# Optimization experiments

Measured on AMD Instinct MI355X. Metric: run time of the kernel, lower is better.

## Reference

```python
import jax, jax.numpy as jnp
from jax import lax
import numpy as np

B, T, NCLS, D = 64, 2048, 20, 2048
LCS_LEN, FSD_LEN = 64, 32
LAMB1, LAMB2, LAMB3 = 1.0, 5e-5, 8e-5
LAMB_LCS, LAMB_FSD = 0.01, 0.01
FEAT_MARGIN = 50.0
THRES = 0.5
GAMMA = 0.1


def cos_sim(a, b):
    a = a / jnp.linalg.norm(a, axis=1, keepdims=True)
    b = b / jnp.linalg.norm(b, axis=1, keepdims=True)
    return a @ b.T


def dp_fsd(c0, c1):
    # soft-LCS/DTW-style recurrence with maxGamma (soft max) over 3 neighbors
    h = c0.shape[-1] // 2
    m = cos_sim(c0[:, :h], c1[:, :h])  # [L, L]
    g = cos_sim(c0[:, h:], c1[:, h:])  # [L, L]
    L = m.shape[0]

    def row_step(prev_row, mg):
        m_row, g_row = mg
        diag = prev_row[:-1]  # C[i-1, j-1]
        up = prev_row[1:]     # C[i-1, j]

        def col_step(left, xs):  # left = C[i, j-1]
            d, u, mij, gij = xs
            neigh = jnp.stack([d, gij + u, gij + left])
            val = mij + GAMMA * jax.nn.logsumexp(neigh / GAMMA)
            return val, val

        _, row_vals = lax.scan(col_step, jnp.zeros((), m.dtype), (diag, up, m_row, g_row))
        new_row = jnp.concatenate([jnp.zeros((1,), m.dtype), row_vals])
        return new_row, None

    final_row, _ = lax.scan(row_step, jnp.zeros(L + 1, m.dtype), (m, g))
    return final_row[-1]


def dp_lcs(c0, c1):
    s = cos_sim(c0, c1)  # [L, L]
    L = s.shape[0]

    def row_step(prev_row, s_row):
        diag = prev_row[:-1]
        up = prev_row[1:]

        def col_step(left, xs):
            d, u, sij = xs
            val = jnp.where(sij > THRES, d + sij, jnp.maximum(u, left))
            return val, val

        _, row_vals = lax.scan(col_step, jnp.zeros((), s.dtype), (diag, up, s_row))
        return jnp.concatenate([jnp.zeros((1,), s.dtype), row_vals]), None

    final_row, _ = lax.scan(row_step, jnp.zeros(L + 1, s.dtype), s)
    return final_row[-1]


def cls_criterion(p, lab):
    return -jnp.mean(jnp.sum(jnp.log(p + 1e-10) * lab, axis=1))


def forward_once(ai_cls, ac_cls, ab_cls, vlab, att, ai_feat, ac_feat, ab_feat, ai_cas):
    bs = ai_cls.shape[0]
    ones = jnp.ones((bs, 1), ai_cls.dtype)
    zeros = jnp.zeros((bs, 1), ai_cls.dtype)
    inst_lab = jnp.concatenate([vlab, zeros], axis=1)
    cont_lab = jnp.concatenate([vlab, ones], axis=1)
    back_lab = jnp.concatenate([jnp.zeros_like(vlab), ones], axis=1)
    inst_lab = inst_lab / jnp.sum(inst_lab, axis=1, keepdims=True)
    cont_lab = cont_lab / jnp.sum(cont_lab, axis=1, keepdims=True)
    back_lab = back_lab / jnp.sum(back_lab, axis=1, keepdims=True)

    inst_loss = cls_criterion(ai_cls, inst_lab)
    cont_loss = cls_criterion(ac_cls, cont_lab)
    back_loss = cls_criterion(ab_cls, back_lab)

    guide_loss = jnp.mean(jnp.sum(jnp.abs(1.0 - ai_cas[:, :, -1] - lax.stop_gradient(att[:, :, 0])), axis=1))

    n_inst = jnp.linalg.norm(ai_feat, axis=1)
    n_cont = jnp.linalg.norm(ac_feat, axis=1)
    n_back = jnp.linalg.norm(ab_feat, axis=1)
    f1 = jnp.maximum(FEAT_MARGIN - n_inst + n_cont, 0.0)
    f2 = jnp.maximum(FEAT_MARGIN - n_cont + n_back, 0.0)
    f3 = n_back
    feat_loss = jnp.mean((f1 + f2 + f3) ** 2)

    sparse_loss = jnp.mean(jnp.sum(att[:, :, :2], axis=1))

    cls_loss = inst_loss + cont_loss + back_loss  # THUMOS14 weights 1/1/1
    return cls_loss + LAMB1 * guide_loss + LAMB2 * feat_loss + LAMB3 * sparse_loss


def _pair_loss(vals, pair_label):
    bs = vals.shape[0]
    pos = jnp.sum(vals * pair_label)
    neg = jnp.sum(vals * (1.0 - pair_label))
    pos_num = jnp.sum(pair_label)
    neg_num = bs - pos_num
    return neg / (neg_num + 1e-10) - pos / (pos_num + 1e-10)


def ftcl_forward(act_inst_cls_0, act_cont_cls_0, act_back_cls_0, vid_label_0, temp_att_0,
                 act_inst_feat_0, act_cont_feat_0, act_back_feat_0, act_inst_cas_0,
                 lcs_candi_0, fsd_act_candi_0, fsd_bak_candi_0,
                 act_inst_cls_1, act_cont_cls_1, act_back_cls_1, vid_label_1, temp_att_1,
                 act_inst_feat_1, act_cont_feat_1, act_back_feat_1, act_inst_cas_1,
                 lcs_candi_1, fsd_act_candi_1, fsd_bak_candi_1):
    loss_0 = forward_once(act_inst_cls_0, act_cont_cls_0, act_back_cls_0, vid_label_0, temp_att_0,
                          act_inst_feat_0, act_cont_feat_0, act_back_feat_0, act_inst_cas_0)
    loss_1 = forward_once(act_inst_cls_1, act_cont_cls_1, act_back_cls_1, vid_label_1, temp_att_1,
                          act_inst_feat_1, act_cont_feat_1, act_back_feat_1, act_inst_cas_1)
    acm_loss = (loss_0 + loss_1) / 2.0

    pair_label = (jnp.sum(vid_label_0 * vid_label_1, axis=1) > 0).astype(jnp.float32)  # [B]

    lcs = jax.vmap(dp_lcs)(lcs_candi_0, lcs_candi_1)  # [B]
    lcs_loss = _pair_loss(lcs, pair_label)

    # pair==1 -> act_1, pair==0 -> bak_1 (matches the per-sample branch in torch)
    fsd_c1 = jnp.where(pair_label[:, None, None] > 0, fsd_act_candi_1, fsd_bak_candi_1)
    fsd = jax.vmap(dp_fsd)(fsd_act_candi_0, fsd_c1)  # [B]
    fsd_loss = _pair_loss(fsd, pair_label)

    return acm_loss + LAMB_LCS * lcs_loss + LAMB_FSD * fsd_loss


def setup_inputs() -> dict:
    key = jax.random.key(0)
    ks = iter(jax.random.split(key, 32))
    rand = lambda s: jax.random.uniform(next(ks), s, jnp.float32)
    randn = lambda s: jax.random.normal(next(ks), s, jnp.float32)
    inp = {}
    for sfx in ('0', '1'):
        inp[f'act_inst_cls_{sfx}'] = rand((B, NCLS + 1))
        inp[f'act_cont_cls_{sfx}'] = rand((B, NCLS + 1))
        inp[f'act_back_cls_{sfx}'] = rand((B, NCLS + 1))
        inp[f'vid_label_{sfx}'] = jnp.ones((B, NCLS), jnp.float32)
        inp[f'temp_att_{sfx}'] = rand((B, T, 3))
        inp[f'act_inst_feat_{sfx}'] = randn((B, D))
        inp[f'act_cont_feat_{sfx}'] = randn((B, D))
        inp[f'act_back_feat_{sfx}'] = randn((B, D))
        inp[f'act_inst_cas_{sfx}'] = rand((B, T, NCLS + 1))
        inp[f'lcs_candi_{sfx}'] = randn((B, LCS_LEN, D))
        inp[f'fsd_act_candi_{sfx}'] = randn((B, FSD_LEN, D))
        inp[f'fsd_bak_candi_{sfx}'] = randn((B, FSD_LEN, D))
    return inp


def reference(act_inst_cls_0, act_cont_cls_0, act_back_cls_0, vid_label_0, temp_att_0,
              act_inst_feat_0, act_cont_feat_0, act_back_feat_0, act_inst_cas_0,
              lcs_candi_0, fsd_act_candi_0, fsd_bak_candi_0,
              act_inst_cls_1, act_cont_cls_1, act_back_cls_1, vid_label_1, temp_att_1,
              act_inst_feat_1, act_cont_feat_1, act_back_feat_1, act_inst_cas_1,
              lcs_candi_1, fsd_act_candi_1, fsd_bak_candi_1):
    return ftcl_forward(act_inst_cls_0, act_cont_cls_0, act_back_cls_0, vid_label_0, temp_att_0,
                        act_inst_feat_0, act_cont_feat_0, act_back_feat_0, act_inst_cas_0,
                        lcs_candi_0, fsd_act_candi_0, fsd_bak_candi_0,
                        act_inst_cls_1, act_cont_cls_1, act_back_cls_1, vid_label_1, temp_att_1,
                        act_inst_feat_1, act_cont_feat_1, act_back_feat_1, act_inst_cas_1,
                        lcs_candi_1, fsd_act_candi_1, fsd_bak_candi_1)
```

## Files before the change

### kernel.cpp

```cpp
#include <hip/hip_runtime.h>
#include <math.h>

#define Bn 64
#define Tn 2048
#define NCLS 20
#define Dn 2048
#define LCSL 64
#define FSDL 32

typedef __bf16 bf16x4 __attribute__((ext_vector_type(4)));
typedef __bf16 bf16x8 __attribute__((ext_vector_type(8)));
typedef float f32x4 __attribute__((ext_vector_type(4)));

#define WS_LCS 0
#define WS_FSD 64
#define WS_NORM 128
#define WS_GS 512
#define WS_LSQ 1024
#define WS_FSQ 66560
#define WS_SPART 99328
#define WS_MG 2196480

__global__ __launch_bounds__(256) void mega_kernel(
    const float* __restrict__ lcs0, const float* __restrict__ lcs1,
    const float* __restrict__ fA0, const float* __restrict__ fA1,
    const float* __restrict__ fB1,
    const float* __restrict__ vid0, const float* __restrict__ vid1,
    const float* __restrict__ cas0, const float* __restrict__ att0,
    const float* __restrict__ cas1, const float* __restrict__ att1,
    const float* __restrict__ f0, const float* __restrict__ f1,
    const float* __restrict__ f2, const float* __restrict__ f3,
    const float* __restrict__ f4, const float* __restrict__ f5,
    float* __restrict__ ws) {
    __shared__ __bf16 tA[4096];
    __shared__ __bf16 tB[4096];
    const int t = threadIdx.x;
    const int bid = blockIdx.x;
    const int w = t >> 6, lane = t & 63;
    const int quad = lane >> 4, l16 = lane & 15;

    if (bid < 512) {
        const int b = bid >> 3, ks = bid & 7;
        const float* c0 = lcs0 + (size_t)b * LCSL * Dn + ks * 256;
        const float* c1 = lcs1 + (size_t)b * LCSL * Dn + ks * 256;

        f32x4 acc[4] = {};
        float sqa[4] = {0.f, 0.f, 0.f, 0.f}, sqb[4] = {0.f, 0.f, 0.f, 0.f};
        float4 pA[4], pB[4];
        #pragma unroll
        for (int l = 0; l < 4; ++l) {
            int idx4 = l * 256 + t;
            int row = idx4 >> 4, kq4 = idx4 & 15;
            pA[l] = *(const float4*)(c0 + (size_t)row * Dn + kq4 * 4);
            pB[l] = *(const float4*)(c1 + (size_t)row * Dn + kq4 * 4);
        }
        for (int kc = 0; kc < 4; ++kc) {
            __syncthreads();
            #pragma unroll
            for (int l = 0; l < 4; ++l) {
                int idx4 = l * 256 + t;
                int row = idx4 >> 4, kq4 = idx4 & 15;
                int c = kq4 >> 1, h = kq4 & 1;
                int pos = row * 64 + ((c ^ (row & 7)) << 3) + h * 4;
                float4 av = pA[l], bv = pB[l];
                bf16x4 a4 = {(__bf16)av.x, (__bf16)av.y, (__bf16)av.z, (__bf16)av.w};
                bf16x4 b4 = {(__bf16)bv.x, (__bf16)bv.y, (__bf16)bv.z, (__bf16)bv.w};
                *(bf16x4*)&tA[pos] = a4;
                *(bf16x4*)&tB[pos] = b4;
                sqa[l] += av.x * av.x + av.y * av.y + av.z * av.z + av.w * av.w;
                sqb[l] += bv.x * bv.x + bv.y * bv.y + bv.z * bv.z + bv.w * bv.w;
            }
            if (kc < 3) {
                const float* n0 = c0 + (kc + 1) * 64;
                const float* n1 = c1 + (kc + 1) * 64;
                #pragma unroll
                for (int l = 0; l < 4; ++l) {
                    int idx4 = l * 256 + t;
                    int row = idx4 >> 4, kq4 = idx4 & 15;
                    pA[l] = *(const float4*)(n0 + (size_t)row * Dn + kq4 * 4);
                    pB[l] = *(const float4*)(n1 + (size_t)row * Dn + kq4 * 4);
                }
            }
            __syncthreads();
            #pragma unroll
            for (int s = 0; s < 2; ++s) {
                int ar = w * 16 + l16;
                int ac_ = (s * 4 + quad) ^ (ar & 7);
                bf16x8 af = *(const bf16x8*)&tA[ar * 64 + (ac_ << 3)];
                #pragma unroll
                for (int tj = 0; tj < 4; ++tj) {
                    int br = tj * 16 + l16;
                    int bc = (s * 4 + quad) ^ (br & 7);
                    bf16x8 bf = *(const bf16x8*)&tB[br * 64 + (bc << 3)];
                    acc[tj] = __builtin_amdgcn_mfma_f32_16x16x32_bf16(af, bf, acc[tj], 0, 0, 0);
                }
            }
        }
        float* dst = ws + WS_SPART + (size_t)(b * 8 + ks) * 4096;
        #pragma unroll
        for (int tj = 0; tj < 4; ++tj)
            #pragma unroll
            for (int rg = 0; rg < 4; ++rg)
                dst[(w * 16 + quad * 4 + rg) * 64 + tj * 16 + l16] = acc[tj][rg];
        #pragma unroll
        for (int l = 0; l < 4; ++l) {
            float sa = sqa[l], sb = sqb[l];
            #pragma unroll
            for (int m = 1; m < 16; m <<= 1) {
                sa += __shfl_xor(sa, m);
                sb += __shfl_xor(sb, m);
            }
            if ((t & 15) == 0) {
                int r = l * 16 + (t >> 4);
                float* q = ws + WS_LSQ + (size_t)(b * 8 + ks) * 128;
                q[r] = sa;
                q[64 + r] = sb;
            }
        }
    } else if (bid < 1024) {
        const int qb = bid - 512;
        const int b = qb >> 3, half = (qb >> 2) & 1, ks = qb & 3;
        float ps = 0.f;
        for (int c = 0; c < NCLS; ++c) ps += vid0[b * NCLS + c] * vid1[b * NCLS + c];
        const float* base1 = (ps > 0.f) ? fA1 : fB1;
        const float* c0 = fA0 + (size_t)b * FSDL * Dn + half * 1024 + ks * 256;
        const float* c1 = base1 + (size_t)b * FSDL * Dn + half * 1024 + ks * 256;
        const int wi = w >> 1, wj = w & 1;

        f32x4 acc = {};
        float sqa[2] = {0.f, 0.f}, sqb[2] = {0.f, 0.f};
        float4 pA[2], pB[2];
        #pragma unroll
        for (int l = 0; l < 2; ++l) {
            int idx4 = l * 256 + t;
            int row = idx4 >> 4, kq4 = idx4 & 15;
            pA[l] = *(const float4*)(c0 + (size_t)row * Dn + kq4 * 4);
            pB[l] = *(const float4*)(c1 + (size_t)row * Dn + kq4 * 4);
        }
        for (int kc = 0; kc < 4; ++kc) {
            __syncthreads();
            #pragma unroll
            for (int l = 0; l < 2; ++l) {
                int idx4 = l * 256 + t;
                int row = idx4 >> 4, kq4 = idx4 & 15;
                int c = kq4 >> 1, h = kq4 & 1;
                int pos = row * 64 + ((c ^ (row & 7)) << 3) + h * 4;
                float4 av = pA[l], bv = pB[l];
                bf16x4 a4 = {(__bf16)av.x, (__bf16)av.y, (__bf16)av.z, (__bf16)av.w};
                bf16x4 b4 = {(__bf16)bv.x, (__bf16)bv.y, (__bf16)bv.z, (__bf16)bv.w};
                *(bf16x4*)&tA[pos] = a4;
                *(bf16x4*)&tB[pos] = b4;
                sqa[l] += av.x * av.x + av.y * av.y + av.z * av.z + av.w * av.w;
                sqb[l] += bv.x * bv.x + bv.y * bv.y + bv.z * bv.z + bv.w * bv.w;
            }
            if (kc < 3) {
                const float* n0 = c0 + (kc + 1) * 64;
                const float* n1 = c1 + (kc + 1) * 64;
                #pragma unroll
                for (int l = 0; l < 2; ++l) {
                    int idx4 = l * 256 + t;
                    int row = idx4 >> 4, kq4 = idx4 & 15;
                    pA[l] = *(const float4*)(n0 + (size_t)row * Dn + kq4 * 4);
                    pB[l] = *(const float4*)(n1 + (size_t)row * Dn + kq4 * 4);
                }
            }
            __syncthreads();
            #pragma unroll
            for (int s = 0; s < 2; ++s) {
                int ar = wi * 16 + l16;
                int ac_ = (s * 4 + quad) ^ (ar & 7);
                bf16x8 af = *(const bf16x8*)&tA[ar * 64 + (ac_ << 3)];
                int br = wj * 16 + l16;
                int bc = (s * 4 + quad) ^ (br & 7);
                bf16x8 bf = *(const bf16x8*)&tB[br * 64 + (bc << 3)];
                acc = __builtin_amdgcn_mfma_f32_16x16x32_bf16(af, bf, acc, 0, 0, 0);
            }
        }
        float* dst = ws + WS_MG + (size_t)((b * 2 + half) * 4 + ks) * 1024;
        #pragma unroll
        for (int rg = 0; rg < 4; ++rg)
            dst[(wi * 16 + quad * 4 + rg) * 32 + wj * 16 + l16] = acc[rg];
        #pragma unroll
        for (int l = 0; l < 2; ++l) {
            float sa = sqa[l], sb = sqb[l];
            #pragma unroll
            for (int m = 1; m < 16; m <<= 1) {
                sa += __shfl_xor(sa, m);
                sb += __shfl_xor(sb, m);
            }
            if ((t & 15) == 0) {
                int r = l * 16 + (t >> 4);
                float* qq = ws + WS_FSQ + (size_t)((b * 2 + half) * 4 + ks) * 64;
                qq[r] = sa;
                qq[32 + r] = sb;
            }
        }
    } else if (bid < 1152) {
        const int gb = bid - 1024;
        const int N = Bn * Tn;
        float g0 = 0.f, s0 = 0.f, g1 = 0.f, s1 = 0.f;
        for (int n = gb * 256 + t; n < 2 * N; n += 128 * 256) {
            int sfx = (n >= N);
            int m = sfx ? (n - N) : n;
            const float* cas = sfx ? cas1 : cas0;
            const float* att = sfx ? att1 : att0;
            float a0 = att[m * 3 + 0];
            float a1 = att[m * 3 + 1];
            float g = fabsf(1.0f - cas[m * (NCLS + 1) + NCLS] - a0);
            float s = a0 + a1;
            if (sfx) { g1 += g; s1 += s; } else { g0 += g; s0 += s; }
        }
        float* red = (float*)tA;
        float vals[4] = {g0, s0, g1, s1};
        #pragma unroll
        for (int v = 0; v < 4; ++v) red[v * 256 + t] = vals[v];
        __syncthreads();
        for (int o = 128; o; o >>= 1) {
            if (t < o) {
                #pragma unroll
                for (int v = 0; v < 4; ++v) red[v * 256 + t] += red[v * 256 + t + o];
            }
            __syncthreads();
        }
        if (t < 4) ws[WS_GS + gb * 4 + t] = red[t * 256];
    } else {
        int R = (bid - 1152) * 4 + w;
        const float* arr[6] = {f0, f1, f2, f3, f4, f5};
        const float* p = arr[R >> 6] + (size_t)(R & 63) * Dn;
        float s = 0.f;
        #pragma unroll
        for (int qd = 0; qd < 8; ++qd) {
            float4 v = *(const float4*)(p + qd * 256 + lane * 4);
            s += v.x * v.x + v.y * v.y + v.z * v.z + v.w * v.w;
        }
        for (int off = 32; off; off >>= 1) s += __shfl_down(s, off);
        if (lane == 0) ws[WS_NORM + R] = sqrtf(s);
    }
}

__global__ __launch_bounds__(256) void dp_kernel(float* __restrict__ ws) {
    const int t = threadIdx.x;
    if (blockIdx.x < 64) {
        const int b = blockIdx.x;
        __shared__ float S[64 * 68];
        __shared__ float inv[128];
        if (t < 128) {
            float s = 0.f;
            #pragma unroll
            for (int ks = 0; ks < 8; ++ks)
                s += ws[WS_LSQ + (size_t)(b * 8 + ks) * 128 + t];
            inv[t] = 1.0f / sqrtf(s);
        }
        __syncthreads();
        const float* sp = ws + WS_SPART + (size_t)b * 32768;
        #pragma unroll
        for (int qd = 0; qd < 4; ++qd) {
            int idx4 = qd * 256 + t;
            int i = idx4 >> 4, j = (idx4 & 15) * 4;
            float4 v = {0.f, 0.f, 0.f, 0.f};
            #pragma unroll
            for (int ks = 0; ks < 8; ++ks) {
                float4 p = *(const float4*)(sp + (size_t)ks * 4096 + idx4 * 4);
                v.x += p.x; v.y += p.y; v.z += p.z; v.w += p.w;
            }
            float ri = inv[i];
            S[i * 68 + j + 0] = v.x * ri * inv[64 + j + 0];
            S[i * 68 + j + 1] = v.y * ri * inv[64 + j + 1];
            S[i * 68 + j + 2] = v.z * ri * inv[64 + j + 2];
            S[i * 68 + j + 3] = v.w * ri * inv[64 + j + 3];
        }
        __syncthreads();
        if (t < 64) {
            float prev = 0.f, prevprev = 0.f;
            float sval_next = S[t * 68 + 0];
            for (int d = 2; d <= 128; ++d) {
                float s = sval_next;
                int jn = d - t - 1;
                if (jn >= 0 && jn < 64) sval_next = S[t * 68 + jn];
                float up = __shfl_up(prev, 1);
                float dg = __shfl_up(prevprev, 1);
                if (t == 0) { up = 0.f; dg = 0.f; }
                int j = d - t - 1;
                float left = prev;
                float val = (s > 0.5f) ? (dg + s) : fmaxf(up, left);
                float cur = (j >= 1 && j <= 64) ? val : 0.f;
                prevprev = prev;
                prev = cur;
            }
            if (t == 63) ws[WS_LCS + b] = prev;
        }
    } else {
        const int b = blockIdx.x - 64;
        __shared__ float M[32 * 36], G[32 * 36];
        __shared__ float inv[128];
        if (t < 128) {
            int half = t >> 6, sub = t & 63;
            float s = 0.f;
            #pragma unroll
            for (int ks = 0; ks < 4; ++ks)
                s += ws[WS_FSQ + (size_t)((b * 2 + half) * 4 + ks) * 64 + sub];
            inv[t] = 1.0f / sqrtf(s);
        }
        __syncthreads();
        {
            int idx4 = t;
            int i = idx4 >> 3, j = (idx4 & 7) * 4;
            float4 vM = {0.f, 0.f, 0.f, 0.f}, vG = {0.f, 0.f, 0.f, 0.f};
            #pragma unroll
            for (int ks = 0; ks < 4; ++ks) {
                float4 pM = *(const float4*)(ws + WS_MG + (size_t)((b * 2 + 0) * 4 + ks) * 1024 + idx4 * 4);
                float4 pG = *(const float4*)(ws + WS_MG + (size_t)((b * 2 + 1) * 4 + ks) * 1024 + idx4 * 4);
                vM.x += pM.x; vM.y += pM.y; vM.z += pM.z; vM.w += pM.w;
                vG.x += pG.x; vG.y += pG.y; vG.z += pG.z; vG.w += pG.w;
            }
            float riM = inv[i], riG = inv[64 + i];
            M[i * 36 + j + 0] = vM.x * riM * inv[32 + j + 0];
            M[i * 36 + j + 1] = vM.y * riM * inv[32 + j + 1];
            M[i * 36 + j + 2] = vM.z * riM * inv[32 + j + 2];
            M[i * 36 + j + 3] = vM.w * riM * inv[32 + j + 3];
            G[i * 36 + j + 0] = vG.x * riG * inv[96 + j + 0];
            G[i * 36 + j + 1] = vG.y * riG * inv[96 + j + 1];
            G[i * 36 + j + 2] = vG.z * riG * inv[96 + j + 2];
            G[i * 36 + j + 3] = vG.w * riG * inv[96 + j + 3];
        }
        __syncthreads();
        if (t < 32) {
            float prev = 0.f, prevprev = 0.f;
            float m_next = M[t * 36 + 0], g_next = G[t * 36 + 0];
            for (int d = 2; d <= 64; ++d) {
                float m = m_next, g = g_next;
                int jn = d - t - 1;
                if (jn >= 0 && jn < 32) { m_next = M[t * 36 + jn]; g_next = G[t * 36 + jn]; }
                float up = __shfl_up(prev, 1);
                float dg = __shfl_up(prevprev, 1);
                if (t == 0) { up = 0.f; dg = 0.f; }
                int j = d - t - 1;
                float left = prev;
                float x0 = dg * 10.0f;
                float x1 = (g + up) * 10.0f;
                float x2 = (g + left) * 10.0f;
                float mx = fmaxf(x0, fmaxf(x1, x2));
                float lse = mx + __logf(__expf(x0 - mx) + __expf(x1 - mx) + __expf(x2 - mx));
                float val = m + 0.1f * lse;
                float cur = (j >= 1 && j <= 32) ? val : 0.f;
                prevprev = prev;
                prev = cur;
            }
            if (t == 31) ws[WS_FSD + b] = prev;
        }
    }
}

__device__ float block_reduce(float v, float* red, int t) {
    red[t] = v;
    __syncthreads();
    for (int o = 128; o; o >>= 1) {
        if (t < o) red[t] += red[t + o];
        __syncthreads();
    }
    float r = red[0];
    __syncthreads();
    return r;
}

__global__ __launch_bounds__(256) void final_kernel(
    const float* __restrict__ ai0, const float* __restrict__ ac0,
    const float* __restrict__ ab0, const float* __restrict__ vid0,
    const float* __restrict__ ai1, const float* __restrict__ ac1,
    const float* __restrict__ ab1, const float* __restrict__ vid1,
    const float* __restrict__ ws, float* __restrict__ out) {
    __shared__ float rs0[Bn], rs1[Bn], plsh[Bn];
    __shared__ float red[256];
    int t = threadIdx.x;
    if (t < Bn) {
        float s0 = 0.f, s1 = 0.f, pp = 0.f;
        for (int c = 0; c < NCLS; ++c) {
            float a = vid0[t * NCLS + c], bl = vid1[t * NCLS + c];
            s0 += a; s1 += bl; pp += a * bl;
        }
        rs0[t] = s0;
        rs1[t] = s1;
        plsh[t] = (pp > 0.f) ? 1.f : 0.f;
    }
    __syncthreads();

    float inst0 = 0.f, cont0 = 0.f, back0 = 0.f;
    float inst1 = 0.f, cont1 = 0.f, back1 = 0.f;
    for (int idx = t; idx < Bn * (NCLS + 1); idx += 256) {
        int b = idx / (NCLS + 1), c = idx % (NCLS + 1);
        float v0 = (c < NCLS) ? vid0[b * NCLS + c] : 0.f;
        float v1 = (c < NCLS) ? vid1[b * NCLS + c] : 0.f;
        float wI0 = (c < NCLS) ? (v0 / rs0[b]) : 0.f;
        float wC0 = ((c < NCLS) ? v0 : 1.f) / (rs0[b] + 1.f);
        float wI1 = (c < NCLS) ? (v1 / rs1[b]) : 0.f;
        float wC1 = ((c < NCLS) ? v1 : 1.f) / (rs1[b] + 1.f);
        inst0 += logf(ai0[idx] + 1e-10f) * wI0;
        cont0 += logf(ac0[idx] + 1e-10f) * wC0;
        inst1 += logf(ai1[idx] + 1e-10f) * wI1;
        cont1 += logf(ac1[idx] + 1e-10f) * wC1;
        if (c == NCLS) {
            back0 += logf(ab0[idx] + 1e-10f);
            back1 += logf(ab1[idx] + 1e-10f);
        }
    }
    float sInst0 = block_reduce(inst0, red, t);
    float sCont0 = block_reduce(cont0, red, t);
    float sBack0 = block_reduce(back0, red, t);
    float sInst1 = block_reduce(inst1, red, t);
    float sCont1 = block_reduce(cont1, red, t);
    float sBack1 = block_reduce(back1, red, t);

    float g0 = 0.f, s0v = 0.f, g1 = 0.f, s1v = 0.f;
    for (int i = t; i < 128; i += 256) {
        g0  += ws[WS_GS + i * 4 + 0];
        s0v += ws[WS_GS + i * 4 + 1];
        g1  += ws[WS_GS + i * 4 + 2];
        s1v += ws[WS_GS + i * 4 + 3];
    }
    float sG0 = block_reduce(g0, red, t);
    float sS0 = block_reduce(s0v, red, t);
    float sG1 = block_reduce(g1, red, t);
    float sS1 = block_reduce(s1v, red, t);

    float fv0 = 0.f, fv1 = 0.f;
    if (t < Bn) {
        const float* nm = ws + WS_NORM;
        {
            float ni = nm[0 * Bn + t], nc = nm[1 * Bn + t], nb = nm[2 * Bn + t];
            float f1 = fmaxf(50.0f - ni + nc, 0.f);
            float f2 = fmaxf(50.0f - nc + nb, 0.f);
            float f = f1 + f2 + nb;
            fv0 = f * f;
        }
        {
            float ni = nm[3 * Bn + t], nc = nm[4 * Bn + t], nb = nm[5 * Bn + t];
            float f1 = fmaxf(50.0f - ni + nc, 0.f);
            float f2 = fmaxf(50.0f - nc + nb, 0.f);
            float f = f1 + f2 + nb;
            fv1 = f * f;
        }
    }
    float sFeat0 = block_reduce(fv0, red, t) / (float)Bn;
    float sFeat1 = block_reduce(fv1, red, t) / (float)Bn;

    float posL = 0.f, negL = 0.f, posF = 0.f, negF = 0.f, pln = 0.f;
    if (t < Bn) {
        float pl = plsh[t];
        float lv = ws[WS_LCS + t];
        float fv = ws[WS_FSD + t];
        posL = lv * pl; negL = lv * (1.f - pl);
        posF = fv * pl; negF = fv * (1.f - pl);
        pln = pl;
    }
    float sPosL = block_reduce(posL, red, t);
    float sNegL = block_reduce(negL, red, t);
    float sPosF = block_reduce(posF, red, t);
    float sNegF = block_reduce(negF, red, t);
    float sPln = block_reduce(pln, red, t);

    if (t == 0) {
        float cls0 = -(sInst0 + sCont0 + sBack0) / (float)Bn;
        float cls1 = -(sInst1 + sCont1 + sBack1) / (float)Bn;
        float guide0 = sG0 / (float)Bn;
        float sparse0 = sS0 / (float)(Bn * 2);
        float guide1 = sG1 / (float)Bn;
        float sparse1 = sS1 / (float)(Bn * 2);
        float loss0 = cls0 + 1.0f * guide0 + 5e-05f * sFeat0 + 8e-05f * sparse0;
        float loss1 = cls1 + 1.0f * guide1 + 5e-05f * sFeat1 + 8e-05f * sparse1;
        float acm = 0.5f * (loss0 + loss1);
        float posn = sPln;
        float negn = (float)Bn - posn;
        float lcs_loss = sNegL / (negn + 1e-10f) - sPosL / (posn + 1e-10f);
        float fsd_loss = sNegF / (negn + 1e-10f) - sPosF / (posn + 1e-10f);
        out[0] = acm + 0.01f * lcs_loss + 0.01f * fsd_loss;
    }
}

extern "C" void kernel_launch(void* const* d_in, const int* in_sizes, int n_in,
                              void* d_out, int out_size, void* d_ws, size_t ws_size,
                              hipStream_t stream) {
    (void)in_sizes; (void)n_in; (void)out_size; (void)ws_size;
    const float* ai0  = (const float*)d_in[0];
    const float* ac0  = (const float*)d_in[1];
    const float* ab0  = (const float*)d_in[2];
    const float* vid0 = (const float*)d_in[3];
    const float* att0 = (const float*)d_in[4];
    const float* fi0  = (const float*)d_in[5];
    const float* fc0  = (const float*)d_in[6];
    const float* fb0  = (const float*)d_in[7];
    const float* cas0 = (const float*)d_in[8];
    const float* lcs0 = (const float*)d_in[9];
    const float* fsdA0 = (const float*)d_in[10];
    const float* ai1  = (const float*)d_in[12];
    const float* ac1  = (const float*)d_in[13];
    const float* ab1  = (const float*)d_in[14];
    const float* vid1 = (const float*)d_in[15];
    const float* att1 = (const float*)d_in[16];
    const float* fi1  = (const float*)d_in[17];
    const float* fc1  = (const float*)d_in[18];
    const float* fb1  = (const float*)d_in[19];
    const float* cas1 = (const float*)d_in[20];
    const float* lcs1 = (const float*)d_in[21];
    const float* fsdA1 = (const float*)d_in[22];
    const float* fsdB1 = (const float*)d_in[23];

    float* ws = (float*)d_ws;

    mega_kernel<<<1248, 256, 0, stream>>>(lcs0, lcs1, fsdA0, fsdA1, fsdB1,
                                          vid0, vid1, cas0, att0, cas1, att1,
                                          fi0, fc0, fb0, fi1, fc1, fb1, ws);
    dp_kernel<<<128, 256, 0, stream>>>(ws);
    final_kernel<<<1, 256, 0, stream>>>(ai0, ac0, ab0, vid0, ai1, ac1, ab1, vid1, ws,
                                        (float*)d_out);
}
```

Measured before the change: 239.5 us.

## Fuse DP and final reduction into main kernel via last-block atomic counters

Merges the three kernel launches into one kernel. Per-batch atomic counters let the last-arriving split-K block run the LCS/FSD dynamic program, and a global counter lets the last block run the final loss reduction. This removes two launch boundaries and lets the DP work overlap with other blocks still running. In exchange it adds a memset launch, threadfences and atomics, and serialises the final reduction on one block at the tail.

```diff
diff --git a/kernel.cpp b/kernel.cpp
--- a/kernel.cpp
+++ b/kernel.cpp
@@ -20,338 +20,9 @@
 #define WS_FSQ 66560
 #define WS_SPART 99328
 #define WS_MG 2196480
-
-__global__ __launch_bounds__(256) void mega_kernel(
-    const float* __restrict__ lcs0, const float* __restrict__ lcs1,
-    const float* __restrict__ fA0, const float* __restrict__ fA1,
-    const float* __restrict__ fB1,
-    const float* __restrict__ vid0, const float* __restrict__ vid1,
-    const float* __restrict__ cas0, const float* __restrict__ att0,
-    const float* __restrict__ cas1, const float* __restrict__ att1,
-    const float* __restrict__ f0, const float* __restrict__ f1,
-    const float* __restrict__ f2, const float* __restrict__ f3,
-    const float* __restrict__ f4, const float* __restrict__ f5,
-    float* __restrict__ ws) {
-    __shared__ __bf16 tA[4096];
-    __shared__ __bf16 tB[4096];
-    const int t = threadIdx.x;
-    const int bid = blockIdx.x;
-    const int w = t >> 6, lane = t & 63;
-    const int quad = lane >> 4, l16 = lane & 15;
-
-    if (bid < 512) {
-        const int b = bid >> 3, ks = bid & 7;
-        const float* c0 = lcs0 + (size_t)b * LCSL * Dn + ks * 256;
-        const float* c1 = lcs1 + (size_t)b * LCSL * Dn + ks * 256;
-
-        f32x4 acc[4] = {};
-        float sqa[4] = {0.f, 0.f, 0.f, 0.f}, sqb[4] = {0.f, 0.f, 0.f, 0.f};
-        float4 pA[4], pB[4];
-        #pragma unroll
-        for (int l = 0; l < 4; ++l) {
-            int idx4 = l * 256 + t;
-            int row = idx4 >> 4, kq4 = idx4 & 15;
-            pA[l] = *(const float4*)(c0 + (size_t)row * Dn + kq4 * 4);
-            pB[l] = *(const float4*)(c1 + (size_t)row * Dn + kq4 * 4);
-        }
-        for (int kc = 0; kc < 4; ++kc) {
-            __syncthreads();
-            #pragma unroll
-            for (int l = 0; l < 4; ++l) {
-                int idx4 = l * 256 + t;
-                int row = idx4 >> 4, kq4 = idx4 & 15;
-                int c = kq4 >> 1, h = kq4 & 1;
-                int pos = row * 64 + ((c ^ (row & 7)) << 3) + h * 4;
-                float4 av = pA[l], bv = pB[l];
-                bf16x4 a4 = {(__bf16)av.x, (__bf16)av.y, (__bf16)av.z, (__bf16)av.w};
-                bf16x4 b4 = {(__bf16)bv.x, (__bf16)bv.y, (__bf16)bv.z, (__bf16)bv.w};
-                *(bf16x4*)&tA[pos] = a4;
-                *(bf16x4*)&tB[pos] = b4;
-                sqa[l] += av.x * av.x + av.y * av.y + av.z * av.z + av.w * av.w;
-                sqb[l] += bv.x * bv.x + bv.y * bv.y + bv.z * bv.z + bv.w * bv.w;
-            }
-            if (kc < 3) {
-                const float* n0 = c0 + (kc + 1) * 64;
-                const float* n1 = c1 + (kc + 1) * 64;
-                #pragma unroll
-                for (int l = 0; l < 4; ++l) {
-                    int idx4 = l * 256 + t;
-                    int row = idx4 >> 4, kq4 = idx4 & 15;
-                    pA[l] = *(const float4*)(n0 + (size_t)row * Dn + kq4 * 4);
-                    pB[l] = *(const float4*)(n1 + (size_t)row * Dn + kq4 * 4);
-                }
-            }
-            __syncthreads();
-            #pragma unroll
-            for (int s = 0; s < 2; ++s) {
-                int ar = w * 16 + l16;
-                int ac_ = (s * 4 + quad) ^ (ar & 7);
-                bf16x8 af = *(const bf16x8*)&tA[ar * 64 + (ac_ << 3)];
-                #pragma unroll
-                for (int tj = 0; tj < 4; ++tj) {
-                    int br = tj * 16 + l16;
-                    int bc = (s * 4 + quad) ^ (br & 7);
-                    bf16x8 bf = *(const bf16x8*)&tB[br * 64 + (bc << 3)];
-                    acc[tj] = __builtin_amdgcn_mfma_f32_16x16x32_bf16(af, bf, acc[tj], 0, 0, 0);
-                }
-            }
-        }
-        float* dst = ws + WS_SPART + (size_t)(b * 8 + ks) * 4096;
-        #pragma unroll
-        for (int tj = 0; tj < 4; ++tj)
-            #pragma unroll
-            for (int rg = 0; rg < 4; ++rg)
-                dst[(w * 16 + quad * 4 + rg) * 64 + tj * 16 + l16] = acc[tj][rg];
-        #pragma unroll
-        for (int l = 0; l < 4; ++l) {
-            float sa = sqa[l], sb = sqb[l];
-            #pragma unroll
-            for (int m = 1; m < 16; m <<= 1) {
-                sa += __shfl_xor(sa, m);
-                sb += __shfl_xor(sb, m);
-            }
-            if ((t & 15) == 0) {
-                int r = l * 16 + (t >> 4);
-                float* q = ws + WS_LSQ + (size_t)(b * 8 + ks) * 128;
-                q[r] = sa;
-                q[64 + r] = sb;
-            }
-        }
-    } else if (bid < 1024) {
-        const int qb = bid - 512;
-        const int b = qb >> 3, half = (qb >> 2) & 1, ks = qb & 3;
-        float ps = 0.f;
-        for (int c = 0; c < NCLS; ++c) ps += vid0[b * NCLS + c] * vid1[b * NCLS + c];
-        const float* base1 = (ps > 0.f) ? fA1 : fB1;
-        const float* c0 = fA0 + (size_t)b * FSDL * Dn + half * 1024 + ks * 256;
-        const float* c1 = base1 + (size_t)b * FSDL * Dn + half * 1024 + ks * 256;
-        const int wi = w >> 1, wj = w & 1;
-
-        f32x4 acc = {};
-        float sqa[2] = {0.f, 0.f}, sqb[2] = {0.f, 0.f};
-        float4 pA[2], pB[2];
-        #pragma unroll
-        for (int l = 0; l < 2; ++l) {
-            int idx4 = l * 256 + t;
-            int row = idx4 >> 4, kq4 = idx4 & 15;
-            pA[l] = *(const float4*)(c0 + (size_t)row * Dn + kq4 * 4);
-            pB[l] = *(const float4*)(c1 + (size_t)row * Dn + kq4 * 4);
-        }
-        for (int kc = 0; kc < 4; ++kc) {
-            __syncthreads();
-            #pragma unroll
-            for (int l = 0; l < 2; ++l) {
-                int idx4 = l * 256 + t;
-                int row = idx4 >> 4, kq4 = idx4 & 15;
-                int c = kq4 >> 1, h = kq4 & 1;
-                int pos = row * 64 + ((c ^ (row & 7)) << 3) + h * 4;
-                float4 av = pA[l], bv = pB[l];
-                bf16x4 a4 = {(__bf16)av.x, (__bf16)av.y, (__bf16)av.z, (__bf16)av.w};
-                bf16x4 b4 = {(__bf16)bv.x, (__bf16)bv.y, (__bf16)bv.z, (__bf16)bv.w};
-                *(bf16x4*)&tA[pos] = a4;
-                *(bf16x4*)&tB[pos] = b4;
-                sqa[l] += av.x * av.x + av.y * av.y + av.z * av.z + av.w * av.w;
-                sqb[l] += bv.x * bv.x + bv.y * bv.y + bv.z * bv.z + bv.w * bv.w;
-            }
-            if (kc < 3) {
-                const float* n0 = c0 + (kc + 1) * 64;
-                const float* n1 = c1 + (kc + 1) * 64;
-                #pragma unroll
-                for (int l = 0; l < 2; ++l) {
-                    int idx4 = l * 256 + t;
-                    int row = idx4 >> 4, kq4 = idx4 & 15;
-                    pA[l] = *(const float4*)(n0 + (size_t)row * Dn + kq4 * 4);
-                    pB[l] = *(const float4*)(n1 + (size_t)row * Dn + kq4 * 4);
-                }
-            }
-            __syncthreads();
-            #pragma unroll
-            for (int s = 0; s < 2; ++s) {
-                int ar = wi * 16 + l16;
-                int ac_ = (s * 4 + quad) ^ (ar & 7);
-                bf16x8 af = *(const bf16x8*)&tA[ar * 64 + (ac_ << 3)];
-                int br = wj * 16 + l16;
-                int bc = (s * 4 + quad) ^ (br & 7);
-                bf16x8 bf = *(const bf16x8*)&tB[br * 64 + (bc << 3)];
-                acc = __builtin_amdgcn_mfma_f32_16x16x32_bf16(af, bf, acc, 0, 0, 0);
-            }
-        }
-        float* dst = ws + WS_MG + (size_t)((b * 2 + half) * 4 + ks) * 1024;
-        #pragma unroll
-        for (int rg = 0; rg < 4; ++rg)
-            dst[(wi * 16 + quad * 4 + rg) * 32 + wj * 16 + l16] = acc[rg];
-        #pragma unroll
-        for (int l = 0; l < 2; ++l) {
-            float sa = sqa[l], sb = sqb[l];
-            #pragma unroll
-            for (int m = 1; m < 16; m <<= 1) {
-                sa += __shfl_xor(sa, m);
-                sb += __shfl_xor(sb, m);
-            }
-            if ((t & 15) == 0) {
-                int r = l * 16 + (t >> 4);
-                float* qq = ws + WS_FSQ + (size_t)((b * 2 + half) * 4 + ks) * 64;
-                qq[r] = sa;
-                qq[32 + r] = sb;
-            }
-        }
-    } else if (bid < 1152) {
-        const int gb = bid - 1024;
-        const int N = Bn * Tn;
-        float g0 = 0.f, s0 = 0.f, g1 = 0.f, s1 = 0.f;
-        for (int n = gb * 256 + t; n < 2 * N; n += 128 * 256) {
-            int sfx = (n >= N);
-            int m = sfx ? (n - N) : n;
-            const float* cas = sfx ? cas1 : cas0;
-            const float* att = sfx ? att1 : att0;
-            float a0 = att[m * 3 + 0];
-            float a1 = att[m * 3 + 1];
-            float g = fabsf(1.0f - cas[m * (NCLS + 1) + NCLS] - a0);
-            float s = a0 + a1;
-            if (sfx) { g1 += g; s1 += s; } else { g0 += g; s0 += s; }
-        }
-        float* red = (float*)tA;
-        float vals[4] = {g0, s0, g1, s1};
-        #pragma unroll
-        for (int v = 0; v < 4; ++v) red[v * 256 + t] = vals[v];
-        __syncthreads();
-        for (int o = 128; o; o >>= 1) {
-            if (t < o) {
-                #pragma unroll
-                for (int v = 0; v < 4; ++v) red[v * 256 + t] += red[v * 256 + t + o];
-            }
-            __syncthreads();
-        }
-        if (t < 4) ws[WS_GS + gb * 4 + t] = red[t * 256];
-    } else {
-        int R = (bid - 1152) * 4 + w;
-        const float* arr[6] = {f0, f1, f2, f3, f4, f5};
-        const float* p = arr[R >> 6] + (size_t)(R & 63) * Dn;
-        float s = 0.f;
-        #pragma unroll
-        for (int qd = 0; qd < 8; ++qd) {
-            float4 v = *(const float4*)(p + qd * 256 + lane * 4);
-            s += v.x * v.x + v.y * v.y + v.z * v.z + v.w * v.w;
-        }
-        for (int off = 32; off; off >>= 1) s += __shfl_down(s, off);
-        if (lane == 0) ws[WS_NORM + R] = sqrtf(s);
-    }
-}
-
-__global__ __launch_bounds__(256) void dp_kernel(float* __restrict__ ws) {
-    const int t = threadIdx.x;
-    if (blockIdx.x < 64) {
-        const int b = blockIdx.x;
-        __shared__ float S[64 * 68];
-        __shared__ float inv[128];
-        if (t < 128) {
-            float s = 0.f;
-            #pragma unroll
-            for (int ks = 0; ks < 8; ++ks)
-                s += ws[WS_LSQ + (size_t)(b * 8 + ks) * 128 + t];
-            inv[t] = 1.0f / sqrtf(s);
-        }
-        __syncthreads();
-        const float* sp = ws + WS_SPART + (size_t)b * 32768;
-        #pragma unroll
-        for (int qd = 0; qd < 4; ++qd) {
-            int idx4 = qd * 256 + t;
-            int i = idx4 >> 4, j = (idx4 & 15) * 4;
-            float4 v = {0.f, 0.f, 0.f, 0.f};
-            #pragma unroll
-            for (int ks = 0; ks < 8; ++ks) {
-                float4 p = *(const float4*)(sp + (size_t)ks * 4096 + idx4 * 4);
-                v.x += p.x; v.y += p.y; v.z += p.z; v.w += p.w;
-            }
-            float ri = inv[i];
-            S[i * 68 + j + 0] = v.x * ri * inv[64 + j + 0];
-            S[i * 68 + j + 1] = v.y * ri * inv[64 + j + 1];
-            S[i * 68 + j + 2] = v.z * ri * inv[64 + j + 2];
-            S[i * 68 + j + 3] = v.w * ri * inv[64 + j + 3];
-        }
-        __syncthreads();
-        if (t < 64) {
-            float prev = 0.f, prevprev = 0.f;
-            float sval_next = S[t * 68 + 0];
-            for (int d = 2; d <= 128; ++d) {
-                float s = sval_next;
-                int jn = d - t - 1;
-                if (jn >= 0 && jn < 64) sval_next = S[t * 68 + jn];
-                float up = __shfl_up(prev, 1);
-                float dg = __shfl_up(prevprev, 1);
-                if (t == 0) { up = 0.f; dg = 0.f; }
-                int j = d - t - 1;
-                float left = prev;
-                float val = (s > 0.5f) ? (dg + s) : fmaxf(up, left);
-                float cur = (j >= 1 && j <= 64) ? val : 0.f;
-                prevprev = prev;
-                prev = cur;
-            }
-            if (t == 63) ws[WS_LCS + b] = prev;
-        }
-    } else {
-        const int b = blockIdx.x - 64;
-        __shared__ float M[32 * 36], G[32 * 36];
-        __shared__ float inv[128];
-        if (t < 128) {
-            int half = t >> 6, sub = t & 63;
-            float s = 0.f;
-            #pragma unroll
-            for (int ks = 0; ks < 4; ++ks)
-                s += ws[WS_FSQ + (size_t)((b * 2 + half) * 4 + ks) * 64 + sub];
-            inv[t] = 1.0f / sqrtf(s);
-        }
-        __syncthreads();
-        {
-            int idx4 = t;
-            int i = idx4 >> 3, j = (idx4 & 7) * 4;
-            float4 vM = {0.f, 0.f, 0.f, 0.f}, vG = {0.f, 0.f, 0.f, 0.f};
-            #pragma unroll
-            for (int ks = 0; ks < 4; ++ks) {
-                float4 pM = *(const float4*)(ws + WS_MG + (size_t)((b * 2 + 0) * 4 + ks) * 1024 + idx4 * 4);
-                float4 pG = *(const float4*)(ws + WS_MG + (size_t)((b * 2 + 1) * 4 + ks) * 1024 + idx4 * 4);
-                vM.x += pM.x; vM.y += pM.y; vM.z += pM.z; vM.w += pM.w;
-                vG.x += pG.x; vG.y += pG.y; vG.z += pG.z; vG.w += pG.w;
-            }
-            float riM = inv[i], riG = inv[64 + i];
-            M[i * 36 + j + 0] = vM.x * riM * inv[32 + j + 0];
-            M[i * 36 + j + 1] = vM.y * riM * inv[32 + j + 1];
-            M[i * 36 + j + 2] = vM.z * riM * inv[32 + j + 2];
-            M[i * 36 + j + 3] = vM.w * riM * inv[32 + j + 3];
-            G[i * 36 + j + 0] = vG.x * riG * inv[96 + j + 0];
-            G[i * 36 + j + 1] = vG.y * riG * inv[96 + j + 1];
-            G[i * 36 + j + 2] = vG.z * riG * inv[96 + j + 2];
-            G[i * 36 + j + 3] = vG.w * riG * inv[96 + j + 3];
-        }
-        __syncthreads();
-        if (t < 32) {
-            float prev = 0.f, prevprev = 0.f;
-            float m_next = M[t * 36 + 0], g_next = G[t * 36 + 0];
-            for (int d = 2; d <= 64; ++d) {
-                float m = m_next, g = g_next;
-                int jn = d - t - 1;
-                if (jn >= 0 && jn < 32) { m_next = M[t * 36 + jn]; g_next = G[t * 36 + jn]; }
-                float up = __shfl_up(prev, 1);
-                float dg = __shfl_up(prevprev, 1);
-                if (t == 0) { up = 0.f; dg = 0.f; }
-                int j = d - t - 1;
-                float left = prev;
-                float x0 = dg * 10.0f;
-                float x1 = (g + up) * 10.0f;
-                float x2 = (g + left) * 10.0f;
-                float mx = fmaxf(x0, fmaxf(x1, x2));
-                float lse = mx + __logf(__expf(x0 - mx) + __expf(x1 - mx) + __expf(x2 - mx));
-                float val = m + 0.1f * lse;
-                float cur = (j >= 1 && j <= 32) ? val : 0.f;
-                prevprev = prev;
-                prev = cur;
-            }
-            if (t == 31) ws[WS_FSD + b] = prev;
-        }
-    }
-}
-
-__device__ float block_reduce(float v, float* red, int t) {
+#define WS_CNT 2720768
+
+__device__ __forceinline__ float block_reduce(float v, float* red, int t) {
     red[t] = v;
     __syncthreads();
     for (int o = 128; o; o >>= 1) {
@@ -363,15 +34,16 @@
     return r;
 }
 
-__global__ __launch_bounds__(256) void final_kernel(
-    const float* __restrict__ ai0, const float* __restrict__ ac0,
-    const float* __restrict__ ab0, const float* __restrict__ vid0,
-    const float* __restrict__ ai1, const float* __restrict__ ac1,
-    const float* __restrict__ ab1, const float* __restrict__ vid1,
-    const float* __restrict__ ws, float* __restrict__ out) {
-    __shared__ float rs0[Bn], rs1[Bn], plsh[Bn];
-    __shared__ float red[256];
-    int t = threadIdx.x;
+__device__ void do_final(const float* __restrict__ ai0, const float* __restrict__ ac0,
+                         const float* __restrict__ ab0, const float* __restrict__ vid0,
+                         const float* __restrict__ ai1, const float* __restrict__ ac1,
+                         const float* __restrict__ ab1, const float* __restrict__ vid1,
+                         const float* __restrict__ ws, float* __restrict__ out,
+                         float* smem, int t) {
+    float* rs0 = smem;
+    float* rs1 = smem + 64;
+    float* plsh = smem + 128;
+    float* red = smem + 192;
     if (t < Bn) {
         float s0 = 0.f, s1 = 0.f, pp = 0.f;
         for (int c = 0; c < NCLS; ++c) {
@@ -473,6 +145,357 @@
         float lcs_loss = sNegL / (negn + 1e-10f) - sPosL / (posn + 1e-10f);
         float fsd_loss = sNegF / (negn + 1e-10f) - sPosF / (posn + 1e-10f);
         out[0] = acm + 0.01f * lcs_loss + 0.01f * fsd_loss;
+    }
+}
+
+__global__ __launch_bounds__(256) void fused_kernel(
+    const float* __restrict__ lcs0, const float* __restrict__ lcs1,
+    const float* __restrict__ fA0, const float* __restrict__ fA1,
+    const float* __restrict__ fB1,
+    const float* __restrict__ vid0, const float* __restrict__ vid1,
+    const float* __restrict__ cas0, const float* __restrict__ att0,
+    const float* __restrict__ cas1, const float* __restrict__ att1,
+    const float* __restrict__ f0, const float* __restrict__ f1,
+    const float* __restrict__ f2, const float* __restrict__ f3,
+    const float* __restrict__ f4, const float* __restrict__ f5,
+    const float* __restrict__ ai0, const float* __restrict__ ac0,
+    const float* __restrict__ ab0, const float* __restrict__ ai1,
+    const float* __restrict__ ac1, const float* __restrict__ ab1,
+    float* __restrict__ ws, float* __restrict__ out) {
+    __shared__ __align__(16) float smem[4608];
+    __shared__ int role;
+    __bf16* tA = (__bf16*)smem;
+    __bf16* tB = (__bf16*)(smem + 2048);
+    unsigned* cnt = (unsigned*)(ws + WS_CNT);
+    const int t = threadIdx.x;
+    const int bid = blockIdx.x;
+    const int w = t >> 6, lane = t & 63;
+    const int quad = lane >> 4, l16 = lane & 15;
+
+    if (bid < 512) {
+        const int b = bid >> 3, ks = bid & 7;
+        const float* c0 = lcs0 + (size_t)b * LCSL * Dn + ks * 256;
+        const float* c1 = lcs1 + (size_t)b * LCSL * Dn + ks * 256;
+
+        f32x4 acc[4] = {};
+        float sqa[4] = {0.f, 0.f, 0.f, 0.f}, sqb[4] = {0.f, 0.f, 0.f, 0.f};
+        float4 pA[4], pB[4];
+        #pragma unroll
+        for (int l = 0; l < 4; ++l) {
+            int idx4 = l * 256 + t;
+            int row = idx4 >> 4, kq4 = idx4 & 15;
+            pA[l] = *(const float4*)(c0 + (size_t)row * Dn + kq4 * 4);
+            pB[l] = *(const float4*)(c1 + (size_t)row * Dn + kq4 * 4);
+        }
+        for (int kc = 0; kc < 4; ++kc) {
+            __syncthreads();
+            #pragma unroll
+            for (int l = 0; l < 4; ++l) {
+                int idx4 = l * 256 + t;
+                int row = idx4 >> 4, kq4 = idx4 & 15;
+                int c = kq4 >> 1, h = kq4 & 1;
+                int pos = row * 64 + ((c ^ (row & 7)) << 3) + h * 4;
+                float4 av = pA[l], bv = pB[l];
+                bf16x4 a4 = {(__bf16)av.x, (__bf16)av.y, (__bf16)av.z, (__bf16)av.w};
+                bf16x4 b4 = {(__bf16)bv.x, (__bf16)bv.y, (__bf16)bv.z, (__bf16)bv.w};
+                *(bf16x4*)&tA[pos] = a4;
+                *(bf16x4*)&tB[pos] = b4;
+                sqa[l] += av.x * av.x + av.y * av.y + av.z * av.z + av.w * av.w;
+                sqb[l] += bv.x * bv.x + bv.y * bv.y + bv.z * bv.z + bv.w * bv.w;
+            }
+            if (kc < 3) {
+                const float* n0 = c0 + (kc + 1) * 64;
+                const float* n1 = c1 + (kc + 1) * 64;
+                #pragma unroll
+                for (int l = 0; l < 4; ++l) {
+                    int idx4 = l * 256 + t;
+                    int row = idx4 >> 4, kq4 = idx4 & 15;
+                    pA[l] = *(const float4*)(n0 + (size_t)row * Dn + kq4 * 4);
+                    pB[l] = *(const float4*)(n1 + (size_t)row * Dn + kq4 * 4);
+                }
+            }
+            __syncthreads();
+            #pragma unroll
+            for (int s = 0; s < 2; ++s) {
+                int ar = w * 16 + l16;
+                int ac_ = (s * 4 + quad) ^ (ar & 7);
+                bf16x8 af = *(const bf16x8*)&tA[ar * 64 + (ac_ << 3)];
+                #pragma unroll
+                for (int tj = 0; tj < 4; ++tj) {
+                    int br = tj * 16 + l16;
+                    int bc = (s * 4 + quad) ^ (br & 7);
+                    bf16x8 bf = *(const bf16x8*)&tB[br * 64 + (bc << 3)];
+                    acc[tj] = __builtin_amdgcn_mfma_f32_16x16x32_bf16(af, bf, acc[tj], 0, 0, 0);
+                }
+            }
+        }
+        float* dst = ws + WS_SPART + (size_t)(b * 8 + ks) * 4096;
+        #pragma unroll
+        for (int tj = 0; tj < 4; ++tj)
+            #pragma unroll
+            for (int rg = 0; rg < 4; ++rg)
+                dst[(w * 16 + quad * 4 + rg) * 64 + tj * 16 + l16] = acc[tj][rg];
+        #pragma unroll
+        for (int l = 0; l < 4; ++l) {
+            float sa = sqa[l], sb = sqb[l];
+            #pragma unroll
+            for (int m = 1; m < 16; m <<= 1) {
+                sa += __shfl_xor(sa, m);
+                sb += __shfl_xor(sb, m);
+            }
+            if ((t & 15) == 0) {
+                int r = l * 16 + (t >> 4);
+                float* q = ws + WS_LSQ + (size_t)(b * 8 + ks) * 128;
+                q[r] = sa;
+                q[64 + r] = sb;
+            }
+        }
+        __threadfence();
+        __syncthreads();
+        if (t == 0) role = (atomicAdd(&cnt[b], 1u) == 7u);
+        __syncthreads();
+        if (role) {
+            __threadfence();
+            float* S = smem;
+            float* inv = smem + 4352;
+            if (t < 128) {
+                float s = 0.f;
+                #pragma unroll
+                for (int k2 = 0; k2 < 8; ++k2)
+                    s += ws[WS_LSQ + (size_t)(b * 8 + k2) * 128 + t];
+                inv[t] = 1.0f / sqrtf(s);
+            }
+            __syncthreads();
+            const float* sp = ws + WS_SPART + (size_t)b * 32768;
+            #pragma unroll
+            for (int qd = 0; qd < 4; ++qd) {
+                int idx4 = qd * 256 + t;
+                int i = idx4 >> 4, j = (idx4 & 15) * 4;
+                float4 v = {0.f, 0.f, 0.f, 0.f};
+                #pragma unroll
+                for (int k2 = 0; k2 < 8; ++k2) {
+                    float4 p = *(const float4*)(sp + (size_t)k2 * 4096 + idx4 * 4);
+                    v.x += p.x; v.y += p.y; v.z += p.z; v.w += p.w;
+                }
+                float ri = inv[i];
+                S[i * 68 + j + 0] = v.x * ri * inv[64 + j + 0];
+                S[i * 68 + j + 1] = v.y * ri * inv[64 + j + 1];
+                S[i * 68 + j + 2] = v.z * ri * inv[64 + j + 2];
+                S[i * 68 + j + 3] = v.w * ri * inv[64 + j + 3];
+            }
+            __syncthreads();
+            if (t < 64) {
+                float prev = 0.f, prevprev = 0.f;
+                float sval_next = S[t * 68 + 0];
+                for (int d = 2; d <= 128; ++d) {
+                    float s = sval_next;
+                    int jn = d - t - 1;
+                    if (jn >= 0 && jn < 64) sval_next = S[t * 68 + jn];
+                    float up = __shfl_up(prev, 1);
+                    float dg = __shfl_up(prevprev, 1);
+                    if (t == 0) { up = 0.f; dg = 0.f; }
+                    int j = d - t - 1;
+                    float left = prev;
+                    float val = (s > 0.5f) ? (dg + s) : fmaxf(up, left);
+                    float cur = (j >= 1 && j <= 64) ? val : 0.f;
+                    prevprev = prev;
+                    prev = cur;
+                }
+                if (t == 63) ws[WS_LCS + b] = prev;
+            }
+        }
+    } else if (bid < 1024) {
+        const int qb = bid - 512;
+        const int b = qb >> 3, half = (qb >> 2) & 1, ks = qb & 3;
+        float ps = 0.f;
+        for (int c = 0; c < NCLS; ++c) ps += vid0[b * NCLS + c] * vid1[b * NCLS + c];
+        const float* base1 = (ps > 0.f) ? fA1 : fB1;
+        const float* c0 = fA0 + (size_t)b * FSDL * Dn + half * 1024 + ks * 256;
+        const float* c1 = base1 + (size_t)b * FSDL * Dn + half * 1024 + ks * 256;
+        const int wi = w >> 1, wj = w & 1;
+
+        f32x4 acc = {};
+        float sqa[2] = {0.f, 0.f}, sqb[2] = {0.f, 0.f};
+        float4 pA[2], pB[2];
+        #pragma unroll
+        for (int l = 0; l < 2; ++l) {
+            int idx4 = l * 256 + t;
+            int row = idx4 >> 4, kq4 = idx4 & 15;
+            pA[l] = *(const float4*)(c0 + (size_t)row * Dn + kq4 * 4);
+            pB[l] = *(const float4*)(c1 + (size_t)row * Dn + kq4 * 4);
+        }
+        for (int kc = 0; kc < 4; ++kc) {
+            __syncthreads();
+            #pragma unroll
+            for (int l = 0; l < 2; ++l) {
+                int idx4 = l * 256 + t;
+                int row = idx4 >> 4, kq4 = idx4 & 15;
+                int c = kq4 >> 1, h = kq4 & 1;
+                int pos = row * 64 + ((c ^ (row & 7)) << 3) + h * 4;
+                float4 av = pA[l], bv = pB[l];
+                bf16x4 a4 = {(__bf16)av.x, (__bf16)av.y, (__bf16)av.z, (__bf16)av.w};
+                bf16x4 b4 = {(__bf16)bv.x, (__bf16)bv.y, (__bf16)bv.z, (__bf16)bv.w};
+                *(bf16x4*)&tA[pos] = a4;
+                *(bf16x4*)&tB[pos] = b4;
+                sqa[l] += av.x * av.x + av.y * av.y + av.z * av.z + av.w * av.w;
+                sqb[l] += bv.x * bv.x + bv.y * bv.y + bv.z * bv.z + bv.w * bv.w;
+            }
+            if (kc < 3) {
+                const float* n0 = c0 + (kc + 1) * 64;
+                const float* n1 = c1 + (kc + 1) * 64;
+                #pragma unroll
+                for (int l = 0; l < 2; ++l) {
+                    int idx4 = l * 256 + t;
+                    int row = idx4 >> 4, kq4 = idx4 & 15;
+                    pA[l] = *(const float4*)(n0 + (size_t)row * Dn + kq4 * 4);
+                    pB[l] = *(const float4*)(n1 + (size_t)row * Dn + kq4 * 4);
+                }
+            }
+            __syncthreads();
+            #pragma unroll
+            for (int s = 0; s < 2; ++s) {
+                int ar = wi * 16 + l16;
+                int ac_ = (s * 4 + quad) ^ (ar & 7);
+                bf16x8 af = *(const bf16x8*)&tA[ar * 64 + (ac_ << 3)];
+                int br = wj * 16 + l16;
+                int bc = (s * 4 + quad) ^ (br & 7);
+                bf16x8 bf = *(const bf16x8*)&tB[br * 64 + (bc << 3)];
+                acc = __builtin_amdgcn_mfma_f32_16x16x32_bf16(af, bf, acc, 0, 0, 0);
+            }
+        }
+        float* dst = ws + WS_MG + (size_t)((b * 2 + half) * 4 + ks) * 1024;
+        #pragma unroll
+        for (int rg = 0; rg < 4; ++rg)
+            dst[(wi * 16 + quad * 4 + rg) * 32 + wj * 16 + l16] = acc[rg];
+        #pragma unroll
+        for (int l = 0; l < 2; ++l) {
+            float sa = sqa[l], sb = sqb[l];
+            #pragma unroll
+            for (int m = 1; m < 16; m <<= 1) {
+                sa += __shfl_xor(sa, m);
+                sb += __shfl_xor(sb, m);
+            }
+            if ((t & 15) == 0) {
+                int r = l * 16 + (t >> 4);
+                float* qq = ws + WS_FSQ + (size_t)((b * 2 + half) * 4 + ks) * 64;
+                qq[r] = sa;
+                qq[32 + r] = sb;
+            }
+        }
+        __threadfence();
+        __syncthreads();
+        if (t == 0) role = (atomicAdd(&cnt[64 + b], 1u) == 7u);
+        __syncthreads();
+        if (role) {
+            __threadfence();
+            float* M = smem;
+            float* G = smem + 1152;
+            float* inv = smem + 2304;
+            if (t < 128) {
+                int h2 = t >> 6, sub = t & 63;
+                float s = 0.f;
+                #pragma unroll
+                for (int k2 = 0; k2 < 4; ++k2)
+                    s += ws[WS_FSQ + (size_t)((b * 2 + h2) * 4 + k2) * 64 + sub];
+                inv[t] = 1.0f / sqrtf(s);
+            }
+            __syncthreads();
+            {
+                int idx4 = t;
+                int i = idx4 >> 3, j = (idx4 & 7) * 4;
+                float4 vM = {0.f, 0.f, 0.f, 0.f}, vG = {0.f, 0.f, 0.f, 0.f};
+                #pragma unroll
+                for (int k2 = 0; k2 < 4; ++k2) {
+                    float4 pM = *(const float4*)(ws + WS_MG + (size_t)((b * 2 + 0) * 4 + k2) * 1024 + idx4 * 4);
+                    float4 pG = *(const float4*)(ws + WS_MG + (size_t)((b * 2 + 1) * 4 + k2) * 1024 + idx4 * 4);
+                    vM.x += pM.x; vM.y += pM.y; vM.z += pM.z; vM.w += pM.w;
+                    vG.x += pG.x; vG.y += pG.y; vG.z += pG.z; vG.w += pG.w;
+                }
+                float riM = inv[i], riG = inv[64 + i];
+                M[i * 36 + j + 0] = vM.x * riM * inv[32 + j + 0];
+                M[i * 36 + j + 1] = vM.y * riM * inv[32 + j + 1];
+                M[i * 36 + j + 2] = vM.z * riM * inv[32 + j + 2];
+                M[i * 36 + j + 3] = vM.w * riM * inv[32 + j + 3];
+                G[i * 36 + j + 0] = vG.x * riG * inv[96 + j + 0];
+                G[i * 36 + j + 1] = vG.y * riG * inv[96 + j + 1];
+                G[i * 36 + j + 2] = vG.z * riG * inv[96 + j + 2];
+                G[i * 36 + j + 3] = vG.w * riG * inv[96 + j + 3];
+            }
+            __syncthreads();
+            if (t < 32) {
+                float prev = 0.f, prevprev = 0.f;
+                float m_next = M[t * 36 + 0], g_next = G[t * 36 + 0];
+                for (int d = 2; d <= 64; ++d) {
+                    float m = m_next, g = g_next;
+                    int jn = d - t - 1;
+                    if (jn >= 0 && jn < 32) { m_next = M[t * 36 + jn]; g_next = G[t * 36 + jn]; }
+                    float up = __shfl_up(prev, 1);
+                    float dg = __shfl_up(prevprev, 1);
+                    if (t == 0) { up = 0.f; dg = 0.f; }
+                    int j = d - t - 1;
+                    float left = prev;
+                    float x0 = dg * 10.0f;
+                    float x1 = (g + up) * 10.0f;
+                    float x2 = (g + left) * 10.0f;
+                    float mx = fmaxf(x0, fmaxf(x1, x2));
+                    float lse = mx + __logf(__expf(x0 - mx) + __expf(x1 - mx) + __expf(x2 - mx));
+                    float val = m + 0.1f * lse;
+                    float cur = (j >= 1 && j <= 32) ? val : 0.f;
+                    prevprev = prev;
+                    prev = cur;
+                }
+                if (t == 31) ws[WS_FSD + b] = prev;
+            }
+        }
+    } else if (bid < 1152) {
+        const int gb = bid - 1024;
+        const int N = Bn * Tn;
+        float g0 = 0.f, s0 = 0.f, g1 = 0.f, s1 = 0.f;
+        for (int n = gb * 256 + t; n < 2 * N; n += 128 * 256) {
+            int sfx = (n >= N);
+            int m = sfx ? (n - N) : n;
+            const float* cas = sfx ? cas1 : cas0;
+            const float* att = sfx ? att1 : att0;
+            float a0 = att[m * 3 + 0];
+            float a1 = att[m * 3 + 1];
+            float g = fabsf(1.0f - cas[m * (NCLS + 1) + NCLS] - a0);
+            float s = a0 + a1;
+            if (sfx) { g1 += g; s1 += s; } else { g0 += g; s0 += s; }
+        }
+        float* red = smem;
+        float vals[4] = {g0, s0, g1, s1};
+        #pragma unroll
+        for (int v = 0; v < 4; ++v) red[v * 256 + t] = vals[v];
+        __syncthreads();
+        for (int o = 128; o; o >>= 1) {
+            if (t < o) {
+                #pragma unroll
+                for (int v = 0; v < 4; ++v) red[v * 256 + t] += red[v * 256 + t + o];
+            }
+            __syncthreads();
+        }
+        if (t < 4) ws[WS_GS + gb * 4 + t] = red[t * 256];
+    } else {
+        int R = (bid - 1152) * 4 + w;
+        const float* arr[6] = {f0, f1, f2, f3, f4, f5};
+        const float* p = arr[R >> 6] + (size_t)(R & 63) * Dn;
+        float s = 0.f;
+        #pragma unroll
+        for (int qd = 0; qd < 8; ++qd) {
+            float4 v = *(const float4*)(p + qd * 256 + lane * 4);
+            s += v.x * v.x + v.y * v.y + v.z * v.z + v.w * v.w;
+        }
+        for (int off = 32; off; off >>= 1) s += __shfl_down(s, off);
+        if (lane == 0) ws[WS_NORM + R] = sqrtf(s);
+    }
+
+    __threadfence();
+    __syncthreads();
+    if (t == 0) role = (atomicAdd(&cnt[128], 1u) == 1247u);
+    __syncthreads();
+    if (role) {
+        __threadfence();
+        do_final(ai0, ac0, ab0, vid0, ai1, ac1, ab1, vid1, ws, out, smem, t);
     }
 }
 
@@ -506,10 +529,11 @@
 
     float* ws = (float*)d_ws;
 
-    mega_kernel<<<1248, 256, 0, stream>>>(lcs0, lcs1, fsdA0, fsdA1, fsdB1,
-                                          vid0, vid1, cas0, att0, cas1, att1,
-                                          fi0, fc0, fb0, fi1, fc1, fb1, ws);
-    dp_kernel<<<128, 256, 0, stream>>>(ws);
-    final_kernel<<<1, 256, 0, stream>>>(ai0, ac0, ab0, vid0, ai1, ac1, ab1, vid1, ws,
-                                        (float*)d_out);
+    hipMemsetAsync((char*)d_ws + (size_t)WS_CNT * 4, 0, 129 * sizeof(unsigned), stream);
+
+    fused_kernel<<<1248, 256, 0, stream>>>(lcs0, lcs1, fsdA0, fsdA1, fsdB1,
+                                           vid0, vid1, cas0, att0, cas1, att1,
+                                           fi0, fc0, fb0, fi1, fc1, fb1,
+                                           ai0, ac0, ab0, ai1, ac1, ab1,
+                                           ws, (float*)d_out);
 }
```

Result: slower. 604.5 us (+152.4%).
